# Kernel tuning notes

Measured on AMD Instinct MI355X. Metric: run time of the kernel, lower is better.

## Reference

```python
import jax, jax.numpy as jnp
import numpy as np

BAND_WIDTHS = [16]*20 + [32]*12 + [64]*4 + [65]
B, C, F, T, E = 4, 2, 1025, 2048, 128
MAX_BW = 65
D = C * MAX_BW * 2  # padded feature dim (in_channels * max_bandwidth * reim)
EPS = 1e-5


def _band_meta():
    widths = np.asarray(BAND_WIDTHS, np.int32)
    starts = np.concatenate([[0], np.cumsum(widths)[:-1]]).astype(np.int32)
    nb = len(widths)
    bw_mask = (np.arange(MAX_BW)[None, :] < widths[:, None])  # [nb, MAX_BW]
    # feature order per band is (channel, bw, reim), matching torch view_as_real+reshape
    feat_mask = np.broadcast_to(bw_mask[:, None, :, None], (nb, C, MAX_BW, 2)).reshape(nb, D)
    return starts, widths, feat_mask.astype(np.float32)


def setup_inputs() -> dict:
    key = jax.random.key(0)
    ks = jax.random.split(key, 6)
    starts, widths, feat_mask = _band_meta()
    nb = len(widths)
    fm = jnp.asarray(feat_mask)
    x = jax.random.normal(ks[0], (B, C, F, T, 2), jnp.float32)
    ln_gamma = (1.0 + 0.1 * jax.random.normal(ks[1], (nb, D), jnp.float32)) * fm
    ln_beta = 0.1 * jax.random.normal(ks[2], (nb, D), jnp.float32) * fm
    v = 0.05 * jax.random.normal(ks[3], (nb, E, D), jnp.float32) * fm[:, None, :]
    g = 1.0 + 0.1 * jax.random.normal(ks[4], (nb, E), jnp.float32)
    bias = 0.05 * jax.random.normal(ks[5], (nb, E), jnp.float32)
    return {
        "x": x, "ln_gamma": ln_gamma, "ln_beta": ln_beta, "v": v, "g": g,
        "bias": bias, "band_start": jnp.asarray(starts), "band_width": jnp.asarray(widths),
    }


def reference(x, ln_gamma, ln_beta, v, g, bias, band_start, band_width):
    nb = band_start.shape[0]
    # padded gather of each band's frequency slice
    idx = jnp.clip(band_start[:, None] + jnp.arange(MAX_BW)[None, :], 0, F - 1)  # [nb, MAX_BW]
    xb = jnp.take(x, idx, axis=2)               # [B, C, nb, MAX_BW, T, 2]
    xb = jnp.transpose(xb, (0, 2, 4, 1, 3, 5))  # [B, nb, T, C, MAX_BW, 2]
    xb = xb.reshape(B, nb, T, D)
    bw_mask = (jnp.arange(MAX_BW)[None, :] < band_width[:, None])
    fm = jnp.broadcast_to(bw_mask[:, None, :, None], (nb, C, MAX_BW, 2)).reshape(nb, D).astype(x.dtype)
    m = fm[None, :, None, :]                    # [1, nb, 1, D]
    n = (band_width * C * 2).astype(x.dtype)[None, :, None]  # true norm_in per band
    # masked LayerNorm over the valid (ragged) features of each band
    mean = jnp.sum(xb * m, axis=-1) / n         # [B, nb, T]
    diff = (xb - mean[..., None]) * m
    var = jnp.sum(diff * diff, axis=-1) / n
    xhat = diff * jax.lax.rsqrt(var + EPS)[..., None]
    y = (xhat * ln_gamma[None, :, None, :] + ln_beta[None, :, None, :]) * m
    # weight-normalized Linear: W = g * V / ||V||_row (padded cols of V are zero)
    vnorm = jnp.sqrt(jnp.sum(v * v, axis=-1, keepdims=True))  # [nb, E, 1]
    W = g[..., None] * v / vnorm
    z = jnp.einsum("bntd,ned->bnte", y, W) + bias[:, None, :]  # [B, nb, T, E]
    return z
```

## Files before the change

### kernel.cpp

```cpp
#include <hip/hip_runtime.h>
#include <math.h>

#define NB 37
#define BB 4
#define CC 2
#define FF 1025
#define TT 2048
#define EE 128
#define DD 260
#define EPSF 1e-5f
#define CHS 9
#define XROW 40

typedef short s16x8 __attribute__((ext_vector_type(8)));
typedef float f32x4 __attribute__((ext_vector_type(4)));

__device__ __forceinline__ unsigned short f2bf(float f) {
    unsigned u = __builtin_bit_cast(unsigned, f);
    unsigned r = (u + 0x7FFFu + ((u >> 16) & 1u)) >> 16;
    return (unsigned short)r;
}

__global__ __launch_bounds__(256) void prep_kernel(
    const float* __restrict__ gamma, const float* __restrict__ beta,
    const float* __restrict__ v, const float* __restrict__ g,
    const float* __restrict__ bias, const int* __restrict__ bwidth,
    unsigned short* __restrict__ ATg, float* __restrict__ s1o, float* __restrict__ s2o)
{
    int bid = blockIdx.x;
    int n   = bid >> 4;
    int eg  = bid & 15;
    int tid = threadIdx.x;
    int el  = tid >> 5;
    int kk  = tid & 31;
    int e   = eg * 8 + el;

    int bw    = bwidth[n];
    int Deff  = 4 * bw;
    int twobw = 2 * bw;
    int nCh   = (Deff + 31) >> 5;

    const float* vp = v + (size_t)(n * EE + e) * DD;

    float sq = 0.f;
    for (int d = kk; d < DD; d += 32) { float val = vp[d]; sq = fmaf(val, val, sq); }
    #pragma unroll
    for (int m = 16; m >= 1; m >>= 1) sq += __shfl_xor(sq, m);

    float rv = g[n * EE + e] * rsqrtf(sq);

    float s1 = 0.f, s2 = 0.f;
    unsigned short* Abase = ATg + (size_t)n * CHS * (EE * 32) + e * 32 + kk;
    for (int ch = 0; ch < nCh; ++ch) {
        int k = ch * 32 + kk;
        float a = 0.f;
        if (k < Deff) {
            int d = (k >= twobw) ? (130 + k - twobw) : k;
            float W = rv * vp[d];
            a = gamma[n * DD + d] * W;
            s1 += a;
            s2 = fmaf(beta[n * DD + d], W, s2);
        }
        Abase[(size_t)ch * (EE * 32)] = f2bf(a);
    }
    #pragma unroll
    for (int m = 16; m >= 1; m >>= 1) { s1 += __shfl_xor(s1, m); s2 += __shfl_xor(s2, m); }
    if (kk == 0) {
        s1o[n * EE + e] = s1;
        s2o[n * EE + e] = s2 + bias[n * EE + e];
    }
}

__global__ __launch_bounds__(256) void fused_kernel(
    const float* __restrict__ x, const int* __restrict__ bstart,
    const int* __restrict__ bwidth,
    const unsigned short* __restrict__ ATg, const float* __restrict__ s1a,
    const float* __restrict__ s2a, float* __restrict__ out)
{
    int bid = blockIdx.x;
    int tt  = bid & 15;
    int n   = (bid >> 4) % NB;
    int b   = bid / (16 * NB);
    int t0  = tt * 128;
    int f0  = bstart[n];
    int bw  = bwidth[n];
    int nPairs = 2 * bw;
    int Deff   = 4 * bw;
    int nCh    = (Deff + 31) >> 5;

    int tid  = threadIdx.x;
    int lane = tid & 63;
    int l15  = lane & 15;
    int ksub = lane >> 4;

    __shared__ __align__(16) unsigned short Xs[128 * XROW];
    __shared__ __align__(16) unsigned short As[128 * XROW];
    __shared__ unsigned offP[160];
    __shared__ float psum[256], psq[256], ms[128], rss[128];

    for (int p = tid; p < 160; p += 256) {
        unsigned off = 0xFFFFFFFFu;
        if (p < nPairs) {
            int c = (p >= bw) ? 1 : 0;
            int w = p - c * bw;
            off = (unsigned)(((b * CC + c) * FF + f0 + w) * (TT * 2));
        }
        offP[p] = off;
    }
    __syncthreads();

    int tloc = tid & 127;
    int kc8a = tid >> 7;
    float sAcc = 0.f, qAcc = 0.f;

    int wv    = tid >> 6;
    int twave = (wv >> 1) * 64;
    int ewave = (wv & 1) * 64;

    f32x4 acc[4][4];
    #pragma unroll
    for (int mi = 0; mi < 4; ++mi)
        #pragma unroll
        for (int ni = 0; ni < 4; ++ni)
            acc[mi][ni] = (f32x4){0.f, 0.f, 0.f, 0.f};

    const unsigned short* Abase = ATg + (size_t)n * CHS * (EE * 32);

    for (int ch = 0; ch < nCh; ++ch) {
        unsigned short xv[2][8];
        #pragma unroll
        for (int s = 0; s < 2; ++s) {
            int kc8   = kc8a + 2 * s;
            int pbase = ch * 16 + kc8 * 4;
            #pragma unroll
            for (int j = 0; j < 4; ++j) {
                unsigned off = offP[pbase + j];
                float2 val = make_float2(0.f, 0.f);
                if (off != 0xFFFFFFFFu)
                    val = *reinterpret_cast<const float2*>(
                        x + (size_t)off + (size_t)(t0 + tloc) * 2);
                sAcc += val.x + val.y;
                qAcc = fmaf(val.x, val.x, qAcc);
                qAcc = fmaf(val.y, val.y, qAcc);
                xv[s][2 * j]     = f2bf(val.x);
                xv[s][2 * j + 1] = f2bf(val.y);
            }
        }
        const s16x8* Ag = reinterpret_cast<const s16x8*>(Abase + (size_t)ch * (EE * 32));
        s16x8 av0 = Ag[tid];
        s16x8 av1 = Ag[tid + 256];

        __syncthreads();

        #pragma unroll
        for (int s = 0; s < 2; ++s) {
            int kc8 = kc8a + 2 * s;
            *reinterpret_cast<s16x8*>(&Xs[tloc * XROW + kc8 * 8]) =
                *reinterpret_cast<const s16x8*>(&xv[s][0]);
        }
        {
            int e0 = tid >> 2, kc = tid & 3;
            *reinterpret_cast<s16x8*>(&As[e0 * XROW + kc * 8]) = av0;
            *reinterpret_cast<s16x8*>(&As[(64 + e0) * XROW + kc * 8]) = av1;
        }
        __syncthreads();

        s16x8 af[4], bfr[4];
        #pragma unroll
        for (int mi = 0; mi < 4; ++mi)
            af[mi] = *reinterpret_cast<const s16x8*>(
                &Xs[(twave + mi * 16 + l15) * XROW + ksub * 8]);
        #pragma unroll
        for (int ni = 0; ni < 4; ++ni)
            bfr[ni] = *reinterpret_cast<const s16x8*>(
                &As[(ewave + ni * 16 + l15) * XROW + ksub * 8]);
        #pragma unroll
        for (int mi = 0; mi < 4; ++mi)
            #pragma unroll
            for (int ni = 0; ni < 4; ++ni)
                acc[mi][ni] = __builtin_amdgcn_mfma_f32_16x16x32_bf16(
                    af[mi], bfr[ni], acc[mi][ni], 0, 0, 0);
    }

    psum[tid] = sAcc;
    psq[tid]  = qAcc;
    __syncthreads();
    if (tid < 128) {
        float s = psum[tid] + psum[tid + 128];
        float q = psq[tid] + psq[tid + 128];
        float inv = 1.f / (float)Deff;
        float mean = s * inv;
        float var  = q * inv - mean * mean;
        ms[tid]  = mean;
        rss[tid] = rsqrtf(var + EPSF);
    }
    __syncthreads();

    float s1r[4], s2r[4];
    #pragma unroll
    for (int ni = 0; ni < 4; ++ni) {
        int e = ewave + ni * 16 + l15;
        s1r[ni] = s1a[n * EE + e];
        s2r[ni] = s2a[n * EE + e];
    }
    int rbase = ksub * 4;
    size_t outRow = ((size_t)(b * NB + n)) * TT + t0;
    #pragma unroll
    for (int mi = 0; mi < 4; ++mi) {
        #pragma unroll
        for (int j = 0; j < 4; ++j) {
            int t = twave + mi * 16 + rbase + j;
            float m = ms[t], r = rss[t];
            float* op = out + (outRow + t) * EE;
            #pragma unroll
            for (int ni = 0; ni < 4; ++ni) {
                float zv = fmaf(r, acc[mi][ni][j] - m * s1r[ni], s2r[ni]);
                op[ewave + ni * 16 + l15] = zv;
            }
        }
    }
}

extern "C" void kernel_launch(void* const* d_in, const int* in_sizes, int n_in,
                              void* d_out, int out_size, void* d_ws, size_t ws_size,
                              hipStream_t stream)
{
    const float* x      = (const float*)d_in[0];
    const float* gamma  = (const float*)d_in[1];
    const float* beta   = (const float*)d_in[2];
    const float* v      = (const float*)d_in[3];
    const float* g      = (const float*)d_in[4];
    const float* bias   = (const float*)d_in[5];
    const int*   bstart = (const int*)d_in[6];
    const int*   bwidth = (const int*)d_in[7];
    float* out = (float*)d_out;

    unsigned short* ATg = (unsigned short*)d_ws;
    float* s1  = (float*)(ATg + (size_t)NB * CHS * EE * 32);
    float* s2p = s1 + NB * EE;

    prep_kernel<<<NB * 16, 256, 0, stream>>>(gamma, beta, v, g, bias, bwidth, ATg, s1, s2p);
    fused_kernel<<<BB * NB * 16, 256, 0, stream>>>(x, bstart, bwidth, ATg, s1, s2p, out);
}
```

Baseline: 80.30 us.

## Load MFMA fragments directly from global memory, dropping LDS staging and barriers

The fused kernel no longer stages X and the weight tile through shared memory with two barriers per K-chunk. Each wave now loads its own x rows straight into MFMA A-fragments and its weight fragments straight from global memory. LayerNorm statistics are reduced with wave shuffles instead of a shared-memory reduction, and only the last partial chunk is predicated. The cost is that the two wave pairs sharing a row range each load the same x data (and weights are loaded per wave), raising global and L2 traffic and using less coalesced access patterns.

```diff
diff --git a/kernel.cpp b/kernel.cpp
--- a/kernel.cpp
+++ b/kernel.cpp
@@ -10,7 +10,6 @@
 #define DD 260
 #define EPSF 1e-5f
 #define CHS 9
-#define XROW 40
 
 typedef short s16x8 __attribute__((ext_vector_type(8)));
 typedef float f32x4 __attribute__((ext_vector_type(4)));
@@ -71,6 +70,55 @@
     }
 }
 
+template <bool PRED>
+__device__ __forceinline__ void do_chunk(
+    const float* __restrict__ xt, const unsigned* offP,
+    const s16x8* __restrict__ Ab, int ch, int nPairs, int ksub,
+    f32x4 (&acc)[4][4], float (&sA)[4], float (&qA)[4])
+{
+    s16x8 bfr[4];
+    #pragma unroll
+    for (int ni = 0; ni < 4; ++ni) bfr[ni] = Ab[ch * 512 + ni * 64];
+
+    int pb = ch * 16 + (ksub << 2);
+    unsigned o[4]; bool val[4];
+    #pragma unroll
+    for (int j = 0; j < 4; ++j) {
+        int p = pb + j;
+        val[j] = !PRED || (p < nPairs);
+        o[j] = offP[p];
+    }
+
+    #pragma unroll
+    for (int mi = 0; mi < 4; ++mi) {
+        float2 vv[4];
+        #pragma unroll
+        for (int j = 0; j < 4; ++j) {
+            vv[j] = make_float2(0.f, 0.f);
+            if (val[j])
+                vv[j] = *reinterpret_cast<const float2*>(xt + o[j] + mi * 32);
+        }
+        float s = sA[mi], q = qA[mi];
+        #pragma unroll
+        for (int j = 0; j < 4; ++j) {
+            s += vv[j].x + vv[j].y;
+            q = fmaf(vv[j].x, vv[j].x, q);
+            q = fmaf(vv[j].y, vv[j].y, q);
+        }
+        sA[mi] = s; qA[mi] = q;
+        s16x8 af;
+        #pragma unroll
+        for (int j = 0; j < 4; ++j) {
+            af[2 * j]     = (short)f2bf(vv[j].x);
+            af[2 * j + 1] = (short)f2bf(vv[j].y);
+        }
+        #pragma unroll
+        for (int ni = 0; ni < 4; ++ni)
+            acc[mi][ni] = __builtin_amdgcn_mfma_f32_16x16x32_bf16(
+                af, bfr[ni], acc[mi][ni], 0, 0, 0);
+    }
+}
+
 __global__ __launch_bounds__(256) void fused_kernel(
     const float* __restrict__ x, const int* __restrict__ bstart,
     const int* __restrict__ bwidth,
@@ -86,35 +134,27 @@
     int bw  = bwidth[n];
     int nPairs = 2 * bw;
     int Deff   = 4 * bw;
-    int nCh    = (Deff + 31) >> 5;
 
     int tid  = threadIdx.x;
     int lane = tid & 63;
     int l15  = lane & 15;
     int ksub = lane >> 4;
 
-    __shared__ __align__(16) unsigned short Xs[128 * XROW];
-    __shared__ __align__(16) unsigned short As[128 * XROW];
-    __shared__ unsigned offP[160];
-    __shared__ float psum[256], psq[256], ms[128], rss[128];
-
-    for (int p = tid; p < 160; p += 256) {
-        unsigned off = 0xFFFFFFFFu;
-        if (p < nPairs) {
-            int c = (p >= bw) ? 1 : 0;
-            int w = p - c * bw;
+    __shared__ unsigned offP[CHS * 16];
+
+    if (tid < CHS * 16) {
+        unsigned off = 0;
+        if (tid < nPairs) {
+            int c = (tid >= bw) ? 1 : 0;
+            int w = tid - c * bw;
             off = (unsigned)(((b * CC + c) * FF + f0 + w) * (TT * 2));
         }
-        offP[p] = off;
+        offP[tid] = off;
     }
     __syncthreads();
 
-    int tloc = tid & 127;
-    int kc8a = tid >> 7;
-    float sAcc = 0.f, qAcc = 0.f;
-
     int wv    = tid >> 6;
-    int twave = (wv >> 1) * 64;
+    int twave = t0 + (wv >> 1) * 64;
     int ewave = (wv & 1) * 64;
 
     f32x4 acc[4][4];
@@ -123,78 +163,38 @@
         #pragma unroll
         for (int ni = 0; ni < 4; ++ni)
             acc[mi][ni] = (f32x4){0.f, 0.f, 0.f, 0.f};
-
-    const unsigned short* Abase = ATg + (size_t)n * CHS * (EE * 32);
-
-    for (int ch = 0; ch < nCh; ++ch) {
-        unsigned short xv[2][8];
-        #pragma unroll
-        for (int s = 0; s < 2; ++s) {
-            int kc8   = kc8a + 2 * s;
-            int pbase = ch * 16 + kc8 * 4;
-            #pragma unroll
-            for (int j = 0; j < 4; ++j) {
-                unsigned off = offP[pbase + j];
-                float2 val = make_float2(0.f, 0.f);
-                if (off != 0xFFFFFFFFu)
-                    val = *reinterpret_cast<const float2*>(
-                        x + (size_t)off + (size_t)(t0 + tloc) * 2);
-                sAcc += val.x + val.y;
-                qAcc = fmaf(val.x, val.x, qAcc);
-                qAcc = fmaf(val.y, val.y, qAcc);
-                xv[s][2 * j]     = f2bf(val.x);
-                xv[s][2 * j + 1] = f2bf(val.y);
-            }
-        }
-        const s16x8* Ag = reinterpret_cast<const s16x8*>(Abase + (size_t)ch * (EE * 32));
-        s16x8 av0 = Ag[tid];
-        s16x8 av1 = Ag[tid + 256];
-
-        __syncthreads();
-
-        #pragma unroll
-        for (int s = 0; s < 2; ++s) {
-            int kc8 = kc8a + 2 * s;
-            *reinterpret_cast<s16x8*>(&Xs[tloc * XROW + kc8 * 8]) =
-                *reinterpret_cast<const s16x8*>(&xv[s][0]);
-        }
-        {
-            int e0 = tid >> 2, kc = tid & 3;
-            *reinterpret_cast<s16x8*>(&As[e0 * XROW + kc * 8]) = av0;
-            *reinterpret_cast<s16x8*>(&As[(64 + e0) * XROW + kc * 8]) = av1;
-        }
-        __syncthreads();
-
-        s16x8 af[4], bfr[4];
-        #pragma unroll
-        for (int mi = 0; mi < 4; ++mi)
-            af[mi] = *reinterpret_cast<const s16x8*>(
-                &Xs[(twave + mi * 16 + l15) * XROW + ksub * 8]);
-        #pragma unroll
-        for (int ni = 0; ni < 4; ++ni)
-            bfr[ni] = *reinterpret_cast<const s16x8*>(
-                &As[(ewave + ni * 16 + l15) * XROW + ksub * 8]);
-        #pragma unroll
-        for (int mi = 0; mi < 4; ++mi)
-            #pragma unroll
-            for (int ni = 0; ni < 4; ++ni)
-                acc[mi][ni] = __builtin_amdgcn_mfma_f32_16x16x32_bf16(
-                    af[mi], bfr[ni], acc[mi][ni], 0, 0, 0);
-    }
-
-    psum[tid] = sAcc;
-    psq[tid]  = qAcc;
-    __syncthreads();
-    if (tid < 128) {
-        float s = psum[tid] + psum[tid + 128];
-        float q = psq[tid] + psq[tid + 128];
-        float inv = 1.f / (float)Deff;
+    float sA[4] = {0.f, 0.f, 0.f, 0.f};
+    float qA[4] = {0.f, 0.f, 0.f, 0.f};
+
+    const float* xt = x + (size_t)(twave + l15) * 2;
+    const s16x8* Ab = reinterpret_cast<const s16x8*>(
+        ATg + (size_t)n * CHS * (EE * 32) + ((ewave + l15) * 32 + ksub * 8));
+
+    int nChF = Deff >> 5;
+    int rem  = Deff & 31;
+
+    for (int ch = 0; ch < nChF; ++ch)
+        do_chunk<false>(xt, offP, Ab, ch, nPairs, ksub, acc, sA, qA);
+    if (rem)
+        do_chunk<true>(xt, offP, Ab, nChF, nPairs, ksub, acc, sA, qA);
+
+    float inv = 1.f / (float)Deff;
+    float mrow[4][4], rrow[4][4];
+    #pragma unroll
+    for (int mi = 0; mi < 4; ++mi) {
+        float s = sA[mi], q = qA[mi];
+        s += __shfl_xor(s, 16); s += __shfl_xor(s, 32);
+        q += __shfl_xor(q, 16); q += __shfl_xor(q, 32);
         float mean = s * inv;
-        float var  = q * inv - mean * mean;
-        ms[tid]  = mean;
-        rss[tid] = rsqrtf(var + EPSF);
-    }
-    __syncthreads();
+        float var  = fmaf(q, inv, -mean * mean);
+        float rs   = rsqrtf(var + EPSF);
+        #pragma unroll
+        for (int j = 0; j < 4; ++j) {
+            int src = (ksub << 2) + j;
+            mrow[mi][j] = __shfl(mean, src);
+            rrow[mi][j] = __shfl(rs, src);
+        }
+    }
 
     float s1r[4], s2r[4];
     #pragma unroll
@@ -203,20 +203,17 @@
         s1r[ni] = s1a[n * EE + e];
         s2r[ni] = s2a[n * EE + e];
     }
-    int rbase = ksub * 4;
-    size_t outRow = ((size_t)(b * NB + n)) * TT + t0;
+    size_t outRow = ((size_t)(b * NB + n)) * TT;
     #pragma unroll
     for (int mi = 0; mi < 4; ++mi) {
         #pragma unroll
         for (int j = 0; j < 4; ++j) {
-            int t = twave + mi * 16 + rbase + j;
-            float m = ms[t], r = rss[t];
-            float* op = out + (outRow + t) * EE;
+            int t = twave + mi * 16 + (ksub << 2) + j;
+            float m = mrow[mi][j], r = rrow[mi][j];
+            float* op = out + (outRow + t) * EE + ewave + l15;
             #pragma unroll
-            for (int ni = 0; ni < 4; ++ni) {
-                float zv = fmaf(r, acc[mi][ni][j] - m * s1r[ni], s2r[ni]);
-                op[ewave + ni * 16 + l15] = zv;
-            }
+            for (int ni = 0; ni < 4; ++ni)
+                op[ni * 16] = fmaf(r, acc[mi][ni][j] - m * s1r[ni], s2r[ni]);
         }
     }
 }
```

After: 94.23 us. 17.3% more time.
